# Kernel optimization log

Measured on AMD Instinct MI355X. Metric: run time of the kernel, lower is better.

## Reference

```python
import jax, jax.numpy as jnp
import numpy as np

N_Q = 8  # wires in both circuits
EPS = 1e-5
_CNOT = jnp.asarray(np.array([[1, 0, 0, 0], [0, 1, 0, 0], [0, 0, 0, 1], [0, 0, 1, 0]], dtype=np.complex64).reshape(2, 2, 2, 2))


def _rx_gate(theta):
    c = jnp.cos(theta / 2).astype(jnp.complex64)
    s = jnp.sin(theta / 2).astype(jnp.complex64)
    return jnp.stack([jnp.stack([c, -1j * s]), jnp.stack([-1j * s, c])])


def _ry_gate(theta):
    c = jnp.cos(theta / 2).astype(jnp.complex64)
    s = jnp.sin(theta / 2).astype(jnp.complex64)
    return jnp.stack([jnp.stack([c, -s]), jnp.stack([s, c])])


def _apply_1q(state, gate, wire):
    st = jnp.tensordot(gate, state, axes=((1,), (wire,)))
    return jnp.moveaxis(st, 0, wire)


def _apply_cnot(state, ctrl, tgt):
    st = jnp.tensordot(_CNOT, state, axes=((2, 3), (ctrl, tgt)))
    return jnp.moveaxis(st, (0, 1), (ctrl, tgt))


def _measure_z(state, n):
    p = jnp.abs(state) ** 2  # (2,)*n real
    zs = [jnp.take(p, 0, axis=w).sum() - jnp.take(p, 1, axis=w).sum() for w in range(n)]
    return jnp.stack(zs).astype(jnp.float32)


def _init_state(n):
    return jnp.zeros((2,) * n, jnp.complex64).at[(0,) * n].set(1.0)


def _sim_attn_circuit(rx_params):
    # RX(theta_w) on each wire, CNOT ring, <Z> per wire. Encoder is a no-op
    # (torch code calls encoder(qdev) with no data), state starts at |0...0>.
    n = rx_params.shape[0]
    state = _init_state(n)
    for w in range(n):
        state = _apply_1q(state, _rx_gate(rx_params[w]), w)
    for w in range(n - 1):
        state = _apply_cnot(state, w, w + 1)
    state = _apply_cnot(state, n - 1, 0)
    return _measure_z(state, n)


def _sim_ffn_circuit(ry_params):
    n = ry_params.shape[0]
    state = _init_state(n)
    for w in range(n):
        state = _apply_1q(state, _ry_gate(ry_params[w]), w)
    return _measure_z(state, n)


def _layernorm(h, w, b):
    m = h.mean(-1, keepdims=True)
    v = ((h - m) ** 2).mean(-1, keepdims=True)
    return (h - m) * jax.lax.rsqrt(v + EPS) * w + b


def setup_inputs() -> dict:
    key = jax.random.key(0)
    ks = jax.random.split(key, 8)
    B, S, D, F = 64, 8192, 8, 512
    two_pi = 2.0 * np.pi
    return {
        "x": jax.random.normal(ks[0], (B, S, D), jnp.float32),
        "rx_params": jax.random.uniform(ks[1], (N_Q,), jnp.float32) * two_pi,
        "ry_params": jax.random.uniform(ks[2], (N_Q,), jnp.float32) * two_pi,
        "Wc": jax.random.normal(ks[3], (D, D), jnp.float32) / np.sqrt(D),
        "bc": jnp.zeros((D,), jnp.float32),
        "W1": jax.random.normal(ks[4], (F, N_Q), jnp.float32) / np.sqrt(N_Q),
        "b1": jnp.zeros((F,), jnp.float32),
        "W2": jax.random.normal(ks[5], (D, F), jnp.float32) / np.sqrt(F),
        "b2": jnp.zeros((D,), jnp.float32),
        "ln1_w": jnp.ones((D,), jnp.float32),
        "ln1_b": jnp.zeros((D,), jnp.float32),
        "ln2_w": jnp.ones((D,), jnp.float32),
        "ln2_b": jnp.zeros((D,), jnp.float32),
    }


def reference(x, rx_params, ry_params, Wc, bc, W1, b1, W2, b2, ln1_w, ln1_b, ln2_w, ln2_b):
    # Attention branch: circuit output is constant over batch/seq (fresh |0..0>
    # device each position, no data encoding) -> simulate once and broadcast.
    attn_vec = _sim_attn_circuit(rx_params)            # (8,)
    attn_out = attn_vec @ Wc.T + bc                    # (D,) broadcast over (B,S)
    x1 = _layernorm(x + attn_out, ln1_w, ln1_b)        # (B,S,D)
    # FFN branch (dropout is identity in eval): linear2(relu(linear1(qmeas)))
    ffn_vec = _sim_ffn_circuit(ry_params)              # (n_qubits,)
    h = jax.nn.relu(ffn_vec @ W1.T + b1)               # (F,)
    ffn_out = h @ W2.T + b2                            # (D,)
    return _layernorm(x1 + ffn_out, ln2_w, ln2_b)
```

## Files before the change

### kernel.cpp

```cpp
#include <hip/hip_runtime.h>
#include <hip/hip_bf16.h>

typedef float floatx4 __attribute__((ext_vector_type(4)));

__global__ void __launch_bounds__(256) fused_all_kernel(
    const float* __restrict__ x,
    const float* __restrict__ rx, const float* __restrict__ ry,
    const float* __restrict__ Wc, const float* __restrict__ bc,
    const float* __restrict__ W1, const float* __restrict__ b1,
    const float* __restrict__ W2, const float* __restrict__ b2,
    const float* __restrict__ ln1w, const float* __restrict__ ln1b,
    const float* __restrict__ ln2w, const float* __restrict__ ln2b,
    float* __restrict__ out, int nrows)
{
    __shared__ float redm[4][8];
    __shared__ float cvec[16];

    const int t = threadIdx.x;
    const int lane = t & 63;
    const int wv = t >> 6;

    const int rowA = blockIdx.x * 512 + t;
    const int rowB = rowA + 256;
    const bool doA = rowA < nrows;
    const bool doB = rowB < nrows;

    floatx4 xa0 = {0,0,0,0}, xa1 = {0,0,0,0}, xb0 = {0,0,0,0}, xb1 = {0,0,0,0};
    if (doA) {
        const floatx4* p = reinterpret_cast<const floatx4*>(x + (size_t)rowA * 8);
        xa0 = p[0]; xa1 = p[1];
    }
    if (doB) {
        const floatx4* p = reinterpret_cast<const floatx4*>(x + (size_t)rowB * 8);
        xb0 = p[0]; xb1 = p[1];
    }

    float ca[8];
#pragma unroll
    for (int q = 0; q < 8; ++q) ca[q] = cosf(rx[q]);
    float attv[8];
    attv[0] = ca[1] * ca[2] * ca[3] * ca[4] * ca[5] * ca[6] * ca[7];
    {
        float p = ca[0];
#pragma unroll
        for (int k = 1; k < 8; ++k) { p *= ca[k]; attv[k] = p; }
    }

    float fz[8];
#pragma unroll
    for (int q = 0; q < 8; ++q) fz[q] = cosf(ry[q]);

    float acc[8] = {0, 0, 0, 0, 0, 0, 0, 0};
#pragma unroll
    for (int rep = 0; rep < 2; ++rep) {
        const int f = t + rep * 256;
        float hv = b1[f];
#pragma unroll
        for (int q = 0; q < 8; ++q) hv = fmaf(fz[q], W1[f * 8 + q], hv);
        hv = fmaxf(hv, 0.0f);
#pragma unroll
        for (int d = 0; d < 8; ++d) acc[d] = fmaf(hv, W2[d * 512 + f], acc[d]);
    }
#pragma unroll
    for (int off = 32; off >= 1; off >>= 1)
#pragma unroll
        for (int d = 0; d < 8; ++d)
            acc[d] += __shfl_down(acc[d], off);
    if (lane == 0)
#pragma unroll
        for (int d = 0; d < 8; ++d) redm[wv][d] = acc[d];
    __syncthreads();

    if (t < 8) {
        float a = bc[t];
#pragma unroll
        for (int q = 0; q < 8; ++q) a = fmaf(attv[q], Wc[t * 8 + q], a);
        cvec[t] = a;
        cvec[8 + t] = redm[0][t] + redm[1][t] + redm[2][t] + redm[3][t] + b2[t];
    }
    __syncthreads();

    float att[8], ffn[8], w1[8], b1v[8], w2[8], b2v[8];
#pragma unroll
    for (int j = 0; j < 8; ++j) {
        att[j] = cvec[j];
        ffn[j] = cvec[8 + j];
        w1[j] = ln1w[j]; b1v[j] = ln1b[j];
        w2[j] = ln2w[j]; b2v[j] = ln2b[j];
    }

    auto process = [&](floatx4 v0, floatx4 v1, floatx4& o0, floatx4& o1) {
        float h[8] = {v0.x, v0.y, v0.z, v0.w, v1.x, v1.y, v1.z, v1.w};
        float m = 0.0f;
#pragma unroll
        for (int j = 0; j < 8; ++j) { h[j] += att[j]; m += h[j]; }
        m *= 0.125f;
        float v = 0.0f;
#pragma unroll
        for (int j = 0; j < 8; ++j) { const float d = h[j] - m; v = fmaf(d, d, v); }
        v *= 0.125f;
        const float r1 = rsqrtf(v + 1e-5f);

        float g[8];
        float m2 = 0.0f;
#pragma unroll
        for (int j = 0; j < 8; ++j) {
            g[j] = fmaf((h[j] - m) * r1, w1[j], b1v[j]) + ffn[j];
            m2 += g[j];
        }
        m2 *= 0.125f;
        float v2 = 0.0f;
#pragma unroll
        for (int j = 0; j < 8; ++j) { const float d = g[j] - m2; v2 = fmaf(d, d, v2); }
        v2 *= 0.125f;
        const float r2 = rsqrtf(v2 + 1e-5f);

        o0.x = fmaf((g[0] - m2) * r2, w2[0], b2v[0]);
        o0.y = fmaf((g[1] - m2) * r2, w2[1], b2v[1]);
        o0.z = fmaf((g[2] - m2) * r2, w2[2], b2v[2]);
        o0.w = fmaf((g[3] - m2) * r2, w2[3], b2v[3]);
        o1.x = fmaf((g[4] - m2) * r2, w2[4], b2v[4]);
        o1.y = fmaf((g[5] - m2) * r2, w2[5], b2v[5]);
        o1.z = fmaf((g[6] - m2) * r2, w2[6], b2v[6]);
        o1.w = fmaf((g[7] - m2) * r2, w2[7], b2v[7]);
    };

    if (doA) {
        floatx4 o0, o1;
        process(xa0, xa1, o0, o1);
        floatx4* op = reinterpret_cast<floatx4*>(out + (size_t)rowA * 8);
        __builtin_nontemporal_store(o0, op);
        __builtin_nontemporal_store(o1, op + 1);
    }
    if (doB) {
        floatx4 o0, o1;
        process(xb0, xb1, o0, o1);
        floatx4* op = reinterpret_cast<floatx4*>(out + (size_t)rowB * 8);
        __builtin_nontemporal_store(o0, op);
        __builtin_nontemporal_store(o1, op + 1);
    }
}

extern "C" void kernel_launch(void* const* d_in, const int* in_sizes, int n_in,
                              void* d_out, int out_size, void* d_ws, size_t ws_size,
                              hipStream_t stream) {
    const float* x   = (const float*)d_in[0];
    const float* rx  = (const float*)d_in[1];
    const float* ry  = (const float*)d_in[2];
    const float* Wc  = (const float*)d_in[3];
    const float* bc  = (const float*)d_in[4];
    const float* W1  = (const float*)d_in[5];
    const float* b1  = (const float*)d_in[6];
    const float* W2  = (const float*)d_in[7];
    const float* b2  = (const float*)d_in[8];
    const float* ln1w = (const float*)d_in[9];
    const float* ln1b = (const float*)d_in[10];
    const float* ln2w = (const float*)d_in[11];
    const float* ln2b = (const float*)d_in[12];
    float* out = (float*)d_out;

    const int nrows = in_sizes[0] / 8;
    const int blocks = (nrows + 511) / 512;

    fused_all_kernel<<<blocks, 256, 0, stream>>>(
        x, rx, ry, Wc, bc, W1, b1, W2, b2,
        ln1w, ln1b, ln2w, ln2b, out, nrows);
}
```

Before: 13.16 us.

## Use 4 grid-strided rows per thread and per-wave constant reduction without barriers

Each thread now handles four rows strided across the whole grid instead of two adjacent rows, which halves the block count. The FFN constant vector is computed redundantly by every wavefront with an xor-shuffle reduction over all 512 hidden units, so the shared memory and both __syncthreads are gone. Fast __cosf replaces cosf. The aim is to remove block-level synchronization and to spread the constant work over fewer blocks, at the cost of four times more per-wave FFN work and slightly less accurate cosines.

```diff
diff --git a/kernel.cpp b/kernel.cpp
--- a/kernel.cpp
+++ b/kernel.cpp
@@ -13,31 +13,29 @@
     const float* __restrict__ ln2w, const float* __restrict__ ln2b,
     float* __restrict__ out, int nrows)
 {
-    __shared__ float redm[4][8];
-    __shared__ float cvec[16];
-
     const int t = threadIdx.x;
     const int lane = t & 63;
-    const int wv = t >> 6;
+    const int gsize = gridDim.x * 256;
+    const int tid = blockIdx.x * 256 + t;
 
-    const int rowA = blockIdx.x * 512 + t;
-    const int rowB = rowA + 256;
-    const bool doA = rowA < nrows;
-    const bool doB = rowB < nrows;
-
-    floatx4 xa0 = {0,0,0,0}, xa1 = {0,0,0,0}, xb0 = {0,0,0,0}, xb1 = {0,0,0,0};
-    if (doA) {
-        const floatx4* p = reinterpret_cast<const floatx4*>(x + (size_t)rowA * 8);
-        xa0 = p[0]; xa1 = p[1];
-    }
-    if (doB) {
-        const floatx4* p = reinterpret_cast<const floatx4*>(x + (size_t)rowB * 8);
-        xb0 = p[0]; xb1 = p[1];
+    int rows[4];
+    floatx4 xv[4][2];
+#pragma unroll
+    for (int i = 0; i < 4; ++i) {
+        rows[i] = tid + i * gsize;
+        if (rows[i] < nrows) {
+            const floatx4* p = reinterpret_cast<const floatx4*>(x + (size_t)rows[i] * 8);
+            xv[i][0] = p[0];
+            xv[i][1] = p[1];
+        } else {
+            xv[i][0] = (floatx4){0, 0, 0, 0};
+            xv[i][1] = (floatx4){0, 0, 0, 0};
+        }
     }
 
     float ca[8];
 #pragma unroll
-    for (int q = 0; q < 8; ++q) ca[q] = cosf(rx[q]);
+    for (int q = 0; q < 8; ++q) ca[q] = __cosf(rx[q]);
     float attv[8];
     attv[0] = ca[1] * ca[2] * ca[3] * ca[4] * ca[5] * ca[6] * ca[7];
     {
@@ -45,15 +43,14 @@
 #pragma unroll
         for (int k = 1; k < 8; ++k) { p *= ca[k]; attv[k] = p; }
     }
-
     float fz[8];
 #pragma unroll
-    for (int q = 0; q < 8; ++q) fz[q] = cosf(ry[q]);
+    for (int q = 0; q < 8; ++q) fz[q] = __cosf(ry[q]);
 
     float acc[8] = {0, 0, 0, 0, 0, 0, 0, 0};
 #pragma unroll
-    for (int rep = 0; rep < 2; ++rep) {
-        const int f = t + rep * 256;
+    for (int i = 0; i < 8; ++i) {
+        const int f = lane + 64 * i;
         float hv = b1[f];
 #pragma unroll
         for (int q = 0; q < 8; ++q) hv = fmaf(fz[q], W1[f * 8 + q], hv);
@@ -65,28 +62,18 @@
     for (int off = 32; off >= 1; off >>= 1)
 #pragma unroll
         for (int d = 0; d < 8; ++d)
-            acc[d] += __shfl_down(acc[d], off);
-    if (lane == 0)
-#pragma unroll
-        for (int d = 0; d < 8; ++d) redm[wv][d] = acc[d];
-    __syncthreads();
-
-    if (t < 8) {
-        float a = bc[t];
-#pragma unroll
-        for (int q = 0; q < 8; ++q) a = fmaf(attv[q], Wc[t * 8 + q], a);
-        cvec[t] = a;
-        cvec[8 + t] = redm[0][t] + redm[1][t] + redm[2][t] + redm[3][t] + b2[t];
-    }
-    __syncthreads();
+            acc[d] += __shfl_xor(acc[d], off);
 
     float att[8], ffn[8], w1[8], b1v[8], w2[8], b2v[8];
 #pragma unroll
-    for (int j = 0; j < 8; ++j) {
-        att[j] = cvec[j];
-        ffn[j] = cvec[8 + j];
-        w1[j] = ln1w[j]; b1v[j] = ln1b[j];
-        w2[j] = ln2w[j]; b2v[j] = ln2b[j];
+    for (int d = 0; d < 8; ++d) {
+        float a = bc[d];
+#pragma unroll
+        for (int q = 0; q < 8; ++q) a = fmaf(attv[q], Wc[d * 8 + q], a);
+        att[d] = a;
+        ffn[d] = acc[d] + b2[d];
+        w1[d] = ln1w[d]; b1v[d] = ln1b[d];
+        w2[d] = ln2w[d]; b2v[d] = ln2b[d];
     }
 
     auto process = [&](floatx4 v0, floatx4 v1, floatx4& o0, floatx4& o1) {
@@ -125,19 +112,15 @@
         o1.w = fmaf((g[7] - m2) * r2, w2[7], b2v[7]);
     };
 
-    if (doA) {
-        floatx4 o0, o1;
-        process(xa0, xa1, o0, o1);
-        floatx4* op = reinterpret_cast<floatx4*>(out + (size_t)rowA * 8);
-        __builtin_nontemporal_store(o0, op);
-        __builtin_nontemporal_store(o1, op + 1);
-    }
-    if (doB) {
-        floatx4 o0, o1;
-        process(xb0, xb1, o0, o1);
-        floatx4* op = reinterpret_cast<floatx4*>(out + (size_t)rowB * 8);
-        __builtin_nontemporal_store(o0, op);
-        __builtin_nontemporal_store(o1, op + 1);
+#pragma unroll
+    for (int i = 0; i < 4; ++i) {
+        if (rows[i] < nrows) {
+            floatx4 o0, o1;
+            process(xv[i][0], xv[i][1], o0, o1);
+            floatx4* op = reinterpret_cast<floatx4*>(out + (size_t)rows[i] * 8);
+            __builtin_nontemporal_store(o0, op);
+            __builtin_nontemporal_store(o1, op + 1);
+        }
     }
 }
 
@@ -160,7 +143,7 @@
     float* out = (float*)d_out;
 
     const int nrows = in_sizes[0] / 8;
-    const int blocks = (nrows + 511) / 512;
+    const int blocks = (nrows + 4 * 256 - 1) / (4 * 256);
 
     fused_all_kernel<<<blocks, 256, 0, stream>>>(
         x, rx, ry, Wc, bc, W1, b1, W2, b2,
```

After: 13.18 us. No clear change (+0.2%).
